# Kernel tuning notes

Hardware: AMD Instinct MI355X
Metric: run time of the kernel (lower is better)

## Reference

```python
import jax, jax.numpy as jnp
import numpy as np
import math

BS, N, D_MODEL, H = 8, 1024, 512, 8
D_K = D_MODEL // H


def setup_inputs() -> dict:
    key = jax.random.key(0)
    ks = jax.random.split(key, 12)
    s = 1.0 / math.sqrt(D_MODEL)
    inp = {
        "query": jax.random.normal(ks[0], (BS, N, D_MODEL), jnp.float32),
        "key": jax.random.normal(ks[1], (BS, N, D_MODEL), jnp.float32),
        "value": jax.random.normal(ks[2], (BS, N, D_MODEL), jnp.float32),
        "wc_matrix": jax.random.normal(ks[3], (BS, N, N), jnp.float32),
        "Wq": jax.random.normal(ks[4], (D_MODEL, D_MODEL), jnp.float32) * s,
        "bq": jnp.zeros((D_MODEL,), jnp.float32),
        "Wk": jax.random.normal(ks[5], (D_MODEL, D_MODEL), jnp.float32) * s,
        "bk": jnp.zeros((D_MODEL,), jnp.float32),
        "Wv": jax.random.normal(ks[6], (D_MODEL, D_MODEL), jnp.float32) * s,
        "bv": jnp.zeros((D_MODEL,), jnp.float32),
        "Wo": jax.random.normal(ks[7], (D_MODEL, D_MODEL), jnp.float32) * s,
        "bo": jnp.zeros((D_MODEL,), jnp.float32),
    }
    return inp


def _split_heads(x):
    # (bs, N, d_model) -> (bs, h, N, d_k)
    b, n, _ = x.shape
    return x.reshape(b, n, H, D_K).transpose(0, 2, 1, 3)


def reference(query, key, value, wc_matrix, Wq, bq, Wk, bk, Wv, bv, Wo, bo):
    # Linear projections (torch Linear: x @ W.T + b), split into heads
    q = _split_heads(query @ Wq.T + bq)
    k = _split_heads(key @ Wk.T + bk)
    v = _split_heads(value @ Wv.T + bv)

    # scores: (bs, h, N, N)
    scores = jnp.einsum("bhnd,bhmd->bhnm", q, k) / jnp.sqrt(jnp.float32(D_K))
    # WC modulation: scores * softmax(wc)[:, None] + scores  (softmax_wc=True, residual=True)
    wc_sm = jax.nn.softmax(wc_matrix, axis=-1)[:, None]  # (bs, 1, N, N)
    scores = scores * wc_sm + scores
    p_attn = jax.nn.softmax(scores, axis=-1)  # dropout is identity in eval

    a = jnp.einsum("bhnm,bhmd->bhnd", p_attn, v)
    a = a.transpose(0, 2, 1, 3).reshape(query.shape[0], -1, D_MODEL)
    return a @ Wo.T + bo
```

## Files before the change

### kernel.cpp

```cpp
#include <hip/hip_runtime.h>
#include <math.h>


#define BS 8
#define SEQ 1024
#define DM 512
#define NH 8
#define DK 64
#define ROWS (BS * SEQ)

typedef __bf16 bf16_t;
typedef bf16_t bf16x8 __attribute__((ext_vector_type(8)));
typedef bf16_t bf16x4 __attribute__((ext_vector_type(4)));
typedef float f32x4 __attribute__((ext_vector_type(4)));
typedef float f32x16 __attribute__((ext_vector_type(16)));

__device__ inline f32x4 mfma32(bf16x8 a, bf16x8 b, f32x4 c) {
  return __builtin_amdgcn_mfma_f32_16x16x32_bf16(a, b, c, 0, 0, 0);
}
__device__ inline f32x16 mfma3232(bf16x8 a, bf16x8 b, f32x16 c) {
  return __builtin_amdgcn_mfma_f32_32x32x16_bf16(a, b, c, 0, 0, 0);
}

__device__ inline void gload_lds16(const bf16_t* g, bf16_t* l) {
  __builtin_amdgcn_global_load_lds(
      (const __attribute__((address_space(1))) void*)g,
      (__attribute__((address_space(3))) void*)l, 16, 0, 0);
}

__global__ __launch_bounds__(256) void prep_kernel(
    const float* q, const float* k, const float* v,
    const float* wq, const float* wk, const float* wv, const float* wo,
    bf16_t* xq, bf16_t* xk, bf16_t* xv,
    bf16_t* wqb, bf16_t* wkb, bf16_t* wvb, bf16_t* wob,
    const float* __restrict__ wc, bf16_t* __restrict__ G) {
  int bx = blockIdx.x;
  int t = threadIdx.x;
  if (bx < 1664) {
    const float* srcs[7] = {q, k, v, wq, wk, wv, wo};
    bf16_t* dsts[7] = {xq, xk, xv, wqb, wkb, wvb, wob};
    int seg, boff;
    if (bx < 1536) { seg = bx >> 9; boff = bx & 511; }
    else { seg = 3 + ((bx - 1536) >> 5); boff = (bx - 1536) & 31; }
    const float* src = srcs[seg] + (size_t)boff * 8192;
    bf16_t* dst = dsts[seg] + (size_t)boff * 8192;
#pragma unroll
    for (int f = 0; f < 8; ++f) {
      int idx = (f * 256 + t) * 4;
      float4 x = *(const float4*)(src + idx);
      bf16x4 o;
      o[0] = (bf16_t)x.x; o[1] = (bf16_t)x.y; o[2] = (bf16_t)x.z; o[3] = (bf16_t)x.w;
      *(bf16x4*)(dst + idx) = o;
    }
  } else {
    int row = bx - 1664;
    const float* x = wc + (size_t)row * SEQ;
    bf16_t* y = G + (size_t)row * SEQ;
    float4 vv = *(const float4*)(x + t * 4);
    float m = fmaxf(fmaxf(vv.x, vv.y), fmaxf(vv.z, vv.w));
#pragma unroll
    for (int off = 32; off > 0; off >>= 1) m = fmaxf(m, __shfl_xor(m, off, 64));
    __shared__ float sm[4], ss[4];
    int w = t >> 6;
    if ((t & 63) == 0) sm[w] = m;
    __syncthreads();
    m = fmaxf(fmaxf(sm[0], sm[1]), fmaxf(sm[2], sm[3]));
    float4 e;
    e.x = __expf(vv.x - m); e.y = __expf(vv.y - m);
    e.z = __expf(vv.z - m); e.w = __expf(vv.w - m);
    float s = e.x + e.y + e.z + e.w;
#pragma unroll
    for (int off = 32; off > 0; off >>= 1) s += __shfl_xor(s, off, 64);
    if ((t & 63) == 0) ss[w] = s;
    __syncthreads();
    s = ss[0] + ss[1] + ss[2] + ss[3];
    float inv = 1.0f / s;
    const float SC = 0.18033688011112042f;
    bf16x4 g;
    g[0] = (bf16_t)((1.0f + e.x * inv) * SC);
    g[1] = (bf16_t)((1.0f + e.y * inv) * SC);
    g[2] = (bf16_t)((1.0f + e.z * inv) * SC);
    g[3] = (bf16_t)((1.0f + e.w * inv) * SC);
    *(bf16x4*)(y + t * 4) = g;
  }
}

template <int BM, bool OUTF32>
__device__ inline void gemm_core(const bf16_t* X, const bf16_t* W,
                                 const float* bias, void* Cv,
                                 int mblk, int nblk) {
  __shared__ bf16_t As[2][BM * 32];
  __shared__ bf16_t Bs[2][128 * 32];
  int t = threadIdx.x, lane = t & 63, w = t >> 6;
  int quad = lane >> 4, l15 = lane & 15;
  constexpr int MT = BM / 32;
  int m0w = (w & 1) * (BM / 2), n0w = (w >> 1) * 64;
  int mbase = mblk * BM, nbase = nblk * 128;
  int lr = lane >> 2, l4 = lane & 3;
  f32x4 acc[MT][4] = {};

#pragma unroll
  for (int f = 0; f < BM / 64; ++f) {
    int i = f * 4 + w;
    gload_lds16(X + (size_t)(mbase + i * 16 + lr) * DM + l4 * 8, &As[0][i * 512]);
  }
#pragma unroll
  for (int f = 0; f < 2; ++f) {
    int i = f * 4 + w;
    gload_lds16(W + (size_t)(nbase + i * 16 + lr) * DM + l4 * 8, &Bs[0][i * 512]);
  }

  for (int it = 0; it < 16; ++it) {
    __syncthreads();
    int cb = it & 1;
    if (it + 1 < 16) {
      int kb = (it + 1) * 32, nb = (it + 1) & 1;
#pragma unroll
      for (int f = 0; f < BM / 64; ++f) {
        int i = f * 4 + w;
        gload_lds16(X + (size_t)(mbase + i * 16 + lr) * DM + kb + l4 * 8, &As[nb][i * 512]);
      }
#pragma unroll
      for (int f = 0; f < 2; ++f) {
        int i = f * 4 + w;
        gload_lds16(W + (size_t)(nbase + i * 16 + lr) * DM + kb + l4 * 8, &Bs[nb][i * 512]);
      }
    }
    bf16x8 af[MT], bfr[4];
#pragma unroll
    for (int mt = 0; mt < MT; ++mt)
      af[mt] = *(const bf16x8*)&As[cb][(m0w + mt * 16 + l15) * 32 + quad * 8];
#pragma unroll
    for (int nt = 0; nt < 4; ++nt)
      bfr[nt] = *(const bf16x8*)&Bs[cb][(n0w + nt * 16 + l15) * 32 + quad * 8];
#pragma unroll
    for (int mt = 0; mt < MT; ++mt)
#pragma unroll
      for (int nt = 0; nt < 4; ++nt)
        acc[mt][nt] = mfma32(af[mt], bfr[nt], acc[mt][nt]);
  }

#pragma unroll
  for (int nt = 0; nt < 4; ++nt) {
    int col = nbase + n0w + nt * 16 + l15;
    float bc = bias[col];
#pragma unroll
    for (int mt = 0; mt < MT; ++mt)
#pragma unroll
      for (int r = 0; r < 4; ++r) {
        int row = mbase + m0w + mt * 16 + quad * 4 + r;
        float vv = acc[mt][nt][r] + bc;
        if (OUTF32)
          ((float*)Cv)[(size_t)row * DM + col] = vv;
        else
          ((bf16_t*)Cv)[(size_t)row * DM + col] = (bf16_t)vv;
      }
  }
}

__global__ __launch_bounds__(256) void gemm_qkv_kernel(
    const bf16_t* xq, const bf16_t* xk, const bf16_t* xv,
    const bf16_t* wq, const bf16_t* wk, const bf16_t* wv,
    const float* bq, const float* bk, const float* bv,
    bf16_t* cq, bf16_t* ck, bf16_t* cv) {
  const bf16_t* Xarr[3] = {xq, xk, xv};
  const bf16_t* Warr[3] = {wq, wk, wv};
  const float* barr[3] = {bq, bk, bv};
  bf16_t* Carr[3] = {cq, ck, cv};
  int z = blockIdx.z;
  gemm_core<128, false>(Xarr[z], Warr[z], barr[z], Carr[z], blockIdx.x, blockIdx.y);
}

__global__ __launch_bounds__(256) void gemm_wo_kernel(const bf16_t* X, const bf16_t* W,
                                                      const float* bias, float* C) {
  gemm_core<64, true>(X, W, bias, C, blockIdx.x, blockIdx.y);
}

__global__ __launch_bounds__(256) void vtrans_kernel(const bf16_t* __restrict__ Vb,
                                                     bf16_t* __restrict__ Vt) {
  int mt = blockIdx.x;
  int bh = blockIdx.y;
  int b = bh >> 3, h = bh & 7;
  __shared__ bf16_t Ts[64][66];
  int t = threadIdx.x;
#pragma unroll
  for (int f = 0; f < 2; ++f) {
    int chunk = t + f * 256;
    int row = chunk >> 3;
    int c8 = (chunk & 7) * 8;
    bf16x8 v = *(const bf16x8*)&Vb[(size_t)(b * SEQ + mt * 64 + row) * DM + h * DK + c8];
#pragma unroll
    for (int j = 0; j < 8; ++j) Ts[c8 + j][row] = v[j];
  }
  __syncthreads();
#pragma unroll
  for (int f = 0; f < 2; ++f) {
    int chunk = t + f * 256;
    int d = chunk >> 3;
    int m8 = (chunk & 7) * 8;
    bf16x8 o;
#pragma unroll
    for (int j = 0; j < 8; ++j) o[j] = Ts[d][m8 + j];
    *(bf16x8*)&Vt[((size_t)(bh * DK + d)) * SEQ + mt * 64 + m8] = o;
  }
}

__global__ __launch_bounds__(256) void flash_mfma_kernel(
    const bf16_t* __restrict__ Qb, const bf16_t* __restrict__ Kb,
    const bf16_t* __restrict__ Vt, const bf16_t* __restrict__ G,
    bf16_t* __restrict__ Ab) {
  int flat = blockIdx.x + 8 * (blockIdx.y + 8 * blockIdx.z);
  int l = (flat & 7) * 64 + (flat >> 3);
  int qt = l & 7, h = (l >> 3) & 7, b = l >> 6;

  __shared__ bf16_t Ks[2][64 * 64];
  __shared__ bf16_t Vs[2][64 * 64];
  __shared__ bf16_t Ps[4][32 * 64];

  int t = threadIdx.x, lane = t & 63, w = t >> 6;
  int l31 = lane & 31, lh = lane >> 5;
  int s7 = l31 & 7;

  int srow[2], scol[2];
#pragma unroll
  for (int f = 0; f < 2; ++f) {
    int idx = f * 256 + t;
    int r = idx >> 3, p = idx & 7;
    srow[f] = r;
    scol[f] = ((p ^ (r & 7)) * 8);
  }
  const bf16_t* Kbase = Kb + (size_t)(b * SEQ) * DM + h * DK;
  const bf16_t* Vbase = Vt + (size_t)((b * NH + h) * DK) * SEQ;

  size_t qrow_g = (size_t)(b * SEQ + qt * 128 + w * 32 + l31) * DM + h * DK;
  bf16x8 aq[4];
#pragma unroll
  for (int ks = 0; ks < 4; ++ks)
    aq[ks] = *(const bf16x8*)&Qb[qrow_g + ks * 16 + lh * 8];

#pragma unroll
  for (int f = 0; f < 2; ++f) {
    int cbase = (f * 256 + w * 64) * 8;
    gload_lds16(Kbase + (size_t)srow[f] * DM + scol[f], &Ks[0][cbase]);
    gload_lds16(Vbase + (size_t)srow[f] * SEQ + scol[f], &Vs[0][cbase]);
  }
  asm volatile("" ::: "memory");

  const size_t grow = (size_t)(b * SEQ + qt * 128 + w * 32 + l31) * SEQ;
  bf16x4 greg[8];
#pragma unroll
  for (int kt = 0; kt < 2; ++kt)
#pragma unroll
    for (int g4 = 0; g4 < 4; ++g4)
      greg[kt * 4 + g4] = *(const bf16x4*)&G[grow + kt * 32 + g4 * 8 + lh * 4];

  asm volatile("s_waitcnt vmcnt(8)" ::: "memory");
  asm volatile("s_barrier" ::: "memory");

  float l_st = 0.f;
  f32x16 o0 = {}, o1 = {};

  for (int mt = 0; mt < 16; ++mt) {
    int cb = mt & 1;
    if (mt < 15) {
      int nb = cb ^ 1;
      const bf16_t* Kn = Kbase + (size_t)(mt + 1) * 64 * DM;
      const bf16_t* Vn = Vbase + (mt + 1) * 64;
#pragma unroll
      for (int f = 0; f < 2; ++f) {
        int cbase = (f * 256 + w * 64) * 8;
        gload_lds16(Kn + (size_t)srow[f] * DM + scol[f], &Ks[nb][cbase]);
        gload_lds16(Vn + (size_t)srow[f] * SEQ + scol[f], &Vs[nb][cbase]);
      }
      asm volatile("" ::: "memory");
    }

    f32x16 st0 = {}, st1 = {};
    __builtin_amdgcn_s_setprio(1);
#pragma unroll
    for (int ks = 0; ks < 4; ++ks) {
      int c = ((ks * 2 + lh) ^ s7) * 8;
      bf16x8 ak0 = *(const bf16x8*)&Ks[cb][l31 * 64 + c];
      bf16x8 ak1 = *(const bf16x8*)&Ks[cb][(32 + l31) * 64 + c];
      st0 = mfma3232(ak0, aq[ks], st0);
      st1 = mfma3232(ak1, aq[ks], st1);
    }
    __builtin_amdgcn_s_setprio(0);

    float rs = 0.f;
    auto dosm = [&](const f32x16& st, int kt) {
#pragma unroll
      for (int g4 = 0; g4 < 4; ++g4) {
        bf16x4 pb;
#pragma unroll
        for (int rr = 0; rr < 4; ++rr) {
          float p = __builtin_amdgcn_exp2f(st[g4 * 4 + rr] *
                                           (float)greg[kt * 4 + g4][rr]);
          pb[rr] = (bf16_t)p;
          rs += p;
        }
        *(bf16x4*)&Ps[w][l31 * 64 + (((kt * 4 + g4) ^ s7) * 8) + lh * 4] = pb;
      }
    };
    dosm(st0, 0);
    dosm(st1, 1);
    l_st += rs;

    if (mt < 15) {
#pragma unroll
      for (int kt = 0; kt < 2; ++kt)
#pragma unroll
        for (int g4 = 0; g4 < 4; ++g4)
          greg[kt * 4 + g4] = *(const bf16x4*)&G[grow + (mt + 1) * 64 +
                                                 kt * 32 + g4 * 8 + lh * 4];
    }

    __builtin_amdgcn_s_setprio(1);
#pragma unroll
    for (int ks = 0; ks < 4; ++ks) {
      int c = ((ks * 2 + lh) ^ s7) * 8;
      bf16x8 bp = *(const bf16x8*)&Ps[w][l31 * 64 + c];
      bf16x8 av0 = *(const bf16x8*)&Vs[cb][l31 * 64 + c];
      bf16x8 av1 = *(const bf16x8*)&Vs[cb][(32 + l31) * 64 + c];
      o0 = mfma3232(av0, bp, o0);
      o1 = mfma3232(av1, bp, o1);
    }
    __builtin_amdgcn_s_setprio(0);

    if (mt < 15) {
      asm volatile("s_waitcnt vmcnt(8)" ::: "memory");
      asm volatile("s_barrier" ::: "memory");
    }
  }

  l_st += __shfl_xor(l_st, 32, 64);
  float linv = 1.0f / l_st;

#pragma unroll
  for (int dt = 0; dt < 2; ++dt) {
    const f32x16& o = dt ? o1 : o0;
#pragma unroll
    for (int g4 = 0; g4 < 4; ++g4) {
      bf16x4 ov;
#pragma unroll
      for (int rr = 0; rr < 4; ++rr) ov[rr] = (bf16_t)(o[g4 * 4 + rr] * linv);
      *(bf16x4*)&Ab[qrow_g + dt * 32 + g4 * 8 + lh * 4] = ov;
    }
  }
}

extern "C" void kernel_launch(void* const* d_in, const int* in_sizes, int n_in,
                              void* d_out, int out_size, void* d_ws, size_t ws_size,
                              hipStream_t stream) {
  const float* query = (const float*)d_in[0];
  const float* key = (const float*)d_in[1];
  const float* value = (const float*)d_in[2];
  const float* wc = (const float*)d_in[3];
  const float* Wq = (const float*)d_in[4];
  const float* bq = (const float*)d_in[5];
  const float* Wk = (const float*)d_in[6];
  const float* bk = (const float*)d_in[7];
  const float* Wv = (const float*)d_in[8];
  const float* bv = (const float*)d_in[9];
  const float* Wo = (const float*)d_in[10];
  const float* bo = (const float*)d_in[11];
  float* out = (float*)d_out;

  const size_t ACT = (size_t)ROWS * DM;
  const size_t WSZ = (size_t)DM * DM;
  bf16_t* Qb = (bf16_t*)d_ws;
  bf16_t* Kb = Qb + ACT;
  bf16_t* Vb = Kb + ACT;
  bf16_t* Vt = Vb + ACT;
  bf16_t* Ab = Vt + ACT;
  bf16_t* G = Ab + ACT;
  bf16_t* Xq = G + (size_t)BS * SEQ * SEQ;
  bf16_t* Xk = Xq + ACT;
  bf16_t* Xv = Xk + ACT;
  bf16_t* Wqb = Xv + ACT;
  bf16_t* Wkb = Wqb + WSZ;
  bf16_t* Wvb = Wkb + WSZ;
  bf16_t* Wob = Wvb + WSZ;

  prep_kernel<<<1664 + BS * SEQ, 256, 0, stream>>>(
      query, key, value, Wq, Wk, Wv, Wo,
      Xq, Xk, Xv, Wqb, Wkb, Wvb, Wob, wc, G);

  gemm_qkv_kernel<<<dim3(ROWS / 128, DM / 128, 3), 256, 0, stream>>>(
      Xq, Xk, Xv, Wqb, Wkb, Wvb, bq, bk, bv, Qb, Kb, Vb);

  vtrans_kernel<<<dim3(16, 64), 256, 0, stream>>>(Vb, Vt);

  flash_mfma_kernel<<<dim3(SEQ / 128, NH, BS), 256, 0, stream>>>(Qb, Kb, Vt, G, Ab);

  gemm_wo_kernel<<<dim3(ROWS / 64, DM / 128), 256, 0, stream>>>(Ab, Wob, bo, out);
}
```

Measured before the change: 223.2 us.

## Drop LDS staging in flash kernel; keep K/V in registers, permlane P

Removes the shared-memory double buffers for K, V and P. K fragments are loaded straight from global memory into registers with ping-pong prefetch, and V and G are loaded per tile. The P operand for the PV MFMA is rebuilt in registers with packed bf16 conversion and v_permlane32_swap instead of a round-trip through LDS, which also removes the block-wide barriers. The trade-off is more redundant global/L2 traffic, since each wave fetches its own K/V copy, and less latency hiding for V/G loads. Register pressure rises, and launch bounds now request 2 blocks per CU.

```diff
diff --git a/kernel.cpp b/kernel.cpp
--- a/kernel.cpp
+++ b/kernel.cpp
@@ -14,6 +14,8 @@
 typedef bf16_t bf16x4 __attribute__((ext_vector_type(4)));
 typedef float f32x4 __attribute__((ext_vector_type(4)));
 typedef float f32x16 __attribute__((ext_vector_type(16)));
+typedef unsigned int uint32_t_;
+typedef unsigned int uintx4 __attribute__((ext_vector_type(4)));
 
 __device__ inline f32x4 mfma32(bf16x8 a, bf16x8 b, f32x4 c) {
   return __builtin_amdgcn_mfma_f32_16x16x32_bf16(a, b, c, 0, 0, 0);
@@ -26,6 +28,15 @@
   __builtin_amdgcn_global_load_lds(
       (const __attribute__((address_space(1))) void*)g,
       (__attribute__((address_space(3))) void*)l, 16, 0, 0);
+}
+
+__device__ inline unsigned cvtpk_bf16(float lo, float hi) {
+  unsigned d;
+  asm("v_cvt_pk_bf16_f32 %0, %1, %2" : "=v"(d) : "v"(lo), "v"(hi));
+  return d;
+}
+__device__ inline void plswap(unsigned& x, unsigned& y) {
+  asm("v_permlane32_swap_b32 %0, %1" : "+v"(x), "+v"(y));
 }
 
 __global__ __launch_bounds__(256) void prep_kernel(
@@ -205,7 +216,7 @@
   }
 }
 
-__global__ __launch_bounds__(256) void flash_mfma_kernel(
+__global__ __launch_bounds__(256, 2) void flash_mfma_kernel(
     const bf16_t* __restrict__ Qb, const bf16_t* __restrict__ Kb,
     const bf16_t* __restrict__ Vt, const bf16_t* __restrict__ G,
     bf16_t* __restrict__ Ab) {
@@ -213,22 +224,9 @@
   int l = (flat & 7) * 64 + (flat >> 3);
   int qt = l & 7, h = (l >> 3) & 7, b = l >> 6;
 
-  __shared__ bf16_t Ks[2][64 * 64];
-  __shared__ bf16_t Vs[2][64 * 64];
-  __shared__ bf16_t Ps[4][32 * 64];
-
   int t = threadIdx.x, lane = t & 63, w = t >> 6;
   int l31 = lane & 31, lh = lane >> 5;
-  int s7 = l31 & 7;
-
-  int srow[2], scol[2];
-#pragma unroll
-  for (int f = 0; f < 2; ++f) {
-    int idx = f * 256 + t;
-    int r = idx >> 3, p = idx & 7;
-    srow[f] = r;
-    scol[f] = ((p ^ (r & 7)) * 8);
-  }
+
   const bf16_t* Kbase = Kb + (size_t)(b * SEQ) * DM + h * DK;
   const bf16_t* Vbase = Vt + (size_t)((b * NH + h) * DK) * SEQ;
 
@@ -238,99 +236,89 @@
   for (int ks = 0; ks < 4; ++ks)
     aq[ks] = *(const bf16x8*)&Qb[qrow_g + ks * 16 + lh * 8];
 
-#pragma unroll
-  for (int f = 0; f < 2; ++f) {
-    int cbase = (f * 256 + w * 64) * 8;
-    gload_lds16(Kbase + (size_t)srow[f] * DM + scol[f], &Ks[0][cbase]);
-    gload_lds16(Vbase + (size_t)srow[f] * SEQ + scol[f], &Vs[0][cbase]);
-  }
-  asm volatile("" ::: "memory");
-
   const size_t grow = (size_t)(b * SEQ + qt * 128 + w * 32 + l31) * SEQ;
-  bf16x4 greg[8];
-#pragma unroll
-  for (int kt = 0; kt < 2; ++kt)
-#pragma unroll
-    for (int g4 = 0; g4 < 4; ++g4)
-      greg[kt * 4 + g4] = *(const bf16x4*)&G[grow + kt * 32 + g4 * 8 + lh * 4];
-
-  asm volatile("s_waitcnt vmcnt(8)" ::: "memory");
-  asm volatile("s_barrier" ::: "memory");
 
   float l_st = 0.f;
   f32x16 o0 = {}, o1 = {};
 
-  for (int mt = 0; mt < 16; ++mt) {
-    int cb = mt & 1;
-    if (mt < 15) {
-      int nb = cb ^ 1;
-      const bf16_t* Kn = Kbase + (size_t)(mt + 1) * 64 * DM;
-      const bf16_t* Vn = Vbase + (mt + 1) * 64;
-#pragma unroll
-      for (int f = 0; f < 2; ++f) {
-        int cbase = (f * 256 + w * 64) * 8;
-        gload_lds16(Kn + (size_t)srow[f] * DM + scol[f], &Ks[nb][cbase]);
-        gload_lds16(Vn + (size_t)srow[f] * SEQ + scol[f], &Vs[nb][cbase]);
-      }
-      asm volatile("" ::: "memory");
-    }
+  bf16x8 kA[8], kB[8];
+#pragma unroll
+  for (int ks = 0; ks < 4; ++ks) {
+    kA[ks * 2] = *(const bf16x8*)&Kbase[(size_t)(l31)*DM + ks * 16 + lh * 8];
+    kA[ks * 2 + 1] = *(const bf16x8*)&Kbase[(size_t)(32 + l31) * DM + ks * 16 + lh * 8];
+  }
+
+  auto body = [&](int mt, bf16x8(&kU)[8], bf16x8(&kP)[8]) {
+    bf16x8 vf[8];
+#pragma unroll
+    for (int ks = 0; ks < 4; ++ks) {
+      vf[ks * 2] = *(const bf16x8*)&Vbase[(size_t)(l31)*SEQ + mt * 64 + ks * 16 + lh * 8];
+      vf[ks * 2 + 1] =
+          *(const bf16x8*)&Vbase[(size_t)(32 + l31) * SEQ + mt * 64 + ks * 16 + lh * 8];
+    }
+    bf16x4 gr[8];
+#pragma unroll
+    for (int kt = 0; kt < 2; ++kt)
+#pragma unroll
+      for (int g4 = 0; g4 < 4; ++g4)
+        gr[kt * 4 + g4] =
+            *(const bf16x4*)&G[grow + mt * 64 + kt * 32 + g4 * 8 + lh * 4];
 
     f32x16 st0 = {}, st1 = {};
     __builtin_amdgcn_s_setprio(1);
 #pragma unroll
     for (int ks = 0; ks < 4; ++ks) {
-      int c = ((ks * 2 + lh) ^ s7) * 8;
-      bf16x8 ak0 = *(const bf16x8*)&Ks[cb][l31 * 64 + c];
-      bf16x8 ak1 = *(const bf16x8*)&Ks[cb][(32 + l31) * 64 + c];
-      st0 = mfma3232(ak0, aq[ks], st0);
-      st1 = mfma3232(ak1, aq[ks], st1);
+      st0 = mfma3232(kU[ks * 2], aq[ks], st0);
+      st1 = mfma3232(kU[ks * 2 + 1], aq[ks], st1);
     }
     __builtin_amdgcn_s_setprio(0);
 
+    if (mt < 15) {
+      const bf16_t* Kn = Kbase + (size_t)(mt + 1) * 64 * DM;
+#pragma unroll
+      for (int ks = 0; ks < 4; ++ks) {
+        kP[ks * 2] = *(const bf16x8*)&Kn[(size_t)(l31)*DM + ks * 16 + lh * 8];
+        kP[ks * 2 + 1] = *(const bf16x8*)&Kn[(size_t)(32 + l31) * DM + ks * 16 + lh * 8];
+      }
+    }
+
+    float pe0[16], pe1[16];
     float rs = 0.f;
-    auto dosm = [&](const f32x16& st, int kt) {
-#pragma unroll
-      for (int g4 = 0; g4 < 4; ++g4) {
-        bf16x4 pb;
-#pragma unroll
-        for (int rr = 0; rr < 4; ++rr) {
-          float p = __builtin_amdgcn_exp2f(st[g4 * 4 + rr] *
-                                           (float)greg[kt * 4 + g4][rr]);
-          pb[rr] = (bf16_t)p;
-          rs += p;
-        }
-        *(bf16x4*)&Ps[w][l31 * 64 + (((kt * 4 + g4) ^ s7) * 8) + lh * 4] = pb;
-      }
-    };
-    dosm(st0, 0);
-    dosm(st1, 1);
+#pragma unroll
+    for (int g4 = 0; g4 < 4; ++g4)
+#pragma unroll
+      for (int rr = 0; rr < 4; ++rr) {
+        int r = g4 * 4 + rr;
+        float p0 = __builtin_amdgcn_exp2f(st0[r] * (float)gr[g4][rr]);
+        float p1 = __builtin_amdgcn_exp2f(st1[r] * (float)gr[4 + g4][rr]);
+        pe0[r] = p0; pe1[r] = p1;
+        rs += p0 + p1;
+      }
     l_st += rs;
 
-    if (mt < 15) {
-#pragma unroll
-      for (int kt = 0; kt < 2; ++kt)
-#pragma unroll
-        for (int g4 = 0; g4 < 4; ++g4)
-          greg[kt * 4 + g4] = *(const bf16x4*)&G[grow + (mt + 1) * 64 +
-                                                 kt * 32 + g4 * 8 + lh * 4];
-    }
-
     __builtin_amdgcn_s_setprio(1);
 #pragma unroll
     for (int ks = 0; ks < 4; ++ks) {
-      int c = ((ks * 2 + lh) ^ s7) * 8;
-      bf16x8 bp = *(const bf16x8*)&Ps[w][l31 * 64 + c];
-      bf16x8 av0 = *(const bf16x8*)&Vs[cb][l31 * 64 + c];
-      bf16x8 av1 = *(const bf16x8*)&Vs[cb][(32 + l31) * 64 + c];
-      o0 = mfma3232(av0, bp, o0);
-      o1 = mfma3232(av1, bp, o1);
+      const float* pe = (ks < 2) ? pe0 : pe1;
+      int base = (ks & 1) * 8;
+      unsigned d0 = cvtpk_bf16(pe[base + 0], pe[base + 1]);
+      unsigned d1 = cvtpk_bf16(pe[base + 2], pe[base + 3]);
+      unsigned d2 = cvtpk_bf16(pe[base + 4], pe[base + 5]);
+      unsigned d3 = cvtpk_bf16(pe[base + 6], pe[base + 7]);
+      plswap(d0, d2);
+      plswap(d1, d3);
+      uintx4 du = {d0, d1, d2, d3};
+      bf16x8 bp = __builtin_bit_cast(bf16x8, du);
+      o0 = mfma3232(vf[ks * 2], bp, o0);
+      o1 = mfma3232(vf[ks * 2 + 1], bp, o1);
     }
     __builtin_amdgcn_s_setprio(0);
-
-    if (mt < 15) {
-      asm volatile("s_waitcnt vmcnt(8)" ::: "memory");
-      asm volatile("s_barrier" ::: "memory");
-    }
+  };
+
+#pragma unroll 1
+  for (int mt = 0; mt < 16; mt += 2) {
+    body(mt, kA, kB);
+    body(mt + 1, kB, kA);
   }
 
   l_st += __shfl_xor(l_st, 32, 64);
```

New measurement: 263.7 us. 18.2% more time.
